# Kernel tuning notes

Hardware: AMD Instinct MI355X
Metric: run time of the kernel (lower is better)

Reference implementation:

```python
import jax, jax.numpy as jnp
import numpy as np

NHOP = 3

def setup_inputs() -> dict:
    key = jax.random.key(0)
    kq, kk, kv, kw, kb = jax.random.split(key, 5)
    B, Lq, Lk, D = 16, 512, 2048, 1024
    Q = jax.random.normal(kq, (B, Lq, D), dtype=jnp.float32)
    K = jax.random.normal(kk, (B, Lk, D), dtype=jnp.float32)
    V = jax.random.normal(kv, (B, Lk, D), dtype=jnp.float32)
    # nn.Linear(2D, D): weight [D, 2D], bias [D]
    W = jax.random.normal(kw, (D, 2 * D), dtype=jnp.float32) * (1.0 / np.sqrt(2 * D))
    b = jax.random.normal(kb, (D,), dtype=jnp.float32) * 0.01
    return {"Q": Q, "K": K, "V": V, "W": W, "b": b}


def reference(Q, K, V, W, b):
    D = Q.shape[-1]
    scale = 1.0 / jnp.sqrt(jnp.asarray(D, dtype=Q.dtype))
    Q_hop = Q
    attn = None
    for _ in range(NHOP):
        # [B, Lq, Lk]
        scores = jnp.einsum("bqd,bkd->bqk", Q_hop, K) * scale
        attn = jax.nn.softmax(scores, axis=-1)
        R = jnp.einsum("bqk,bkd->bqd", attn, V)          # [B, Lq, D]
        cat = jnp.concatenate([Q_hop, R], axis=-1)       # [B, Lq, 2D]
        Q_hop = jnp.tanh(jnp.einsum("bqe,de->bqd", cat, W) + b)
    return (Q_hop, attn)
```

## Files before the change

### kernel.cpp

```cpp
#include <hip/hip_runtime.h>
#include <math.h>

#define NB 16
#define LQ 512
#define LKK 2048
#define DD 1024

typedef _Float16 half8 __attribute__((ext_vector_type(8)));
typedef _Float16 half4 __attribute__((ext_vector_type(4)));
typedef float f32x4 __attribute__((ext_vector_type(4)));

__device__ __forceinline__ void gl_lds16(const void* g, void* l) {
    __builtin_amdgcn_global_load_lds(
        (const __attribute__((address_space(1))) void*)g,
        (__attribute__((address_space(3))) void*)l, 16, 0, 0);
}

__global__ __launch_bounds__(512, 2) void gemm_qk_256(
    const _Float16* __restrict__ A, long sA,
    const _Float16* __restrict__ B, long sB,
    _Float16* __restrict__ P, long sP,
    float* __restrict__ partial,
    float scale)
{
    __shared__ _Float16 lsA[2][256 * 64];
    __shared__ _Float16 lsB[2][256 * 64];
    const int tid = threadIdx.x;
    const int w = tid >> 6, l = tid & 63;
    const int wr = w >> 2, wc = w & 3;
    const int lrg = l >> 4, lc = l & 15, lr = lrg << 2;

    int id = blockIdx.x + gridDim.x * (blockIdx.y + gridDim.y * blockIdx.z);
    const int nwg = gridDim.x * gridDim.y * gridDim.z;
    id = (id & 7) * (nwg >> 3) + (id >> 3);
    const int bx = id % gridDim.x;
    const int t2 = id / gridDim.x;
    const int by = t2 % gridDim.y;
    const int z  = t2 / gridDim.y;
    const int m0 = by * 256, n0 = bx * 256;

    const _Float16* Ab = A + (size_t)z * sA + (size_t)m0 * DD;
    const _Float16* Bb = B + (size_t)z * sB + (size_t)n0 * DD;

    const int srow = l >> 3;
    const int sk = ((l & 7) ^ srow) << 3;

#define STG(dst, srcbase)                                                     \
    do {                                                                      \
        _Pragma("unroll")                                                     \
        for (int rr = 0; rr < 2; ++rr) {                                      \
            const int c = w + 8 * rr;                                         \
            gl_lds16((srcbase) + (size_t)(c * 8 + srow) * DD + sk,            \
                     (dst) + c * 512);                                        \
        }                                                                     \
    } while (0)

    half8 af[4][2], bf01[2][2], bf23[2][2];
    f32x4 acc[8][4] = {};
    const int rsb = (lc & 7) << 4;

#define LDA(buf, mh)                                                          \
    do {                                                                      \
        const char* p_ = (const char*)lsA[buf];                               \
        _Pragma("unroll")                                                     \
        for (int ii = 0; ii < 4; ++ii) {                                      \
            const int row_ = wr * 128 + (mh) * 64 + ii * 16 + lc;             \
            _Pragma("unroll")                                                 \
            for (int kk = 0; kk < 2; ++kk)                                    \
                af[ii][kk] = *(const half8*)(p_ + row_ * 128 +                \
                             ((kk * 64 + (lrg << 4)) ^ rsb));                 \
        }                                                                     \
    } while (0)

#define LDB(buf, nh, bfr)                                                     \
    do {                                                                      \
        const char* p_ = (const char*)lsB[buf];                               \
        _Pragma("unroll")                                                     \
        for (int jj = 0; jj < 2; ++jj) {                                      \
            const int row_ = wc * 64 + ((nh) * 2 + jj) * 16 + lc;             \
            _Pragma("unroll")                                                 \
            for (int kk = 0; kk < 2; ++kk)                                    \
                bfr[jj][kk] = *(const half8*)(p_ + row_ * 128 +               \
                              ((kk * 64 + (lrg << 4)) ^ rsb));                \
        }                                                                     \
    } while (0)

#define MM(mh, nh, bfr)                                                       \
    do {                                                                      \
        __builtin_amdgcn_s_setprio(1);                                        \
        _Pragma("unroll")                                                     \
        for (int ii = 0; ii < 4; ++ii)                                        \
            _Pragma("unroll")                                                 \
            for (int jj = 0; jj < 2; ++jj)                                    \
                _Pragma("unroll")                                             \
                for (int kk = 0; kk < 2; ++kk)                                \
                    acc[(mh) * 4 + ii][(nh) * 2 + jj] =                       \
                        __builtin_amdgcn_mfma_f32_16x16x32_f16(               \
                            af[ii][kk], bfr[jj][kk],                          \
                            acc[(mh) * 4 + ii][(nh) * 2 + jj], 0, 0, 0);      \
        __builtin_amdgcn_s_setprio(0);                                        \
    } while (0)

#define BAR __builtin_amdgcn_s_barrier()
#define VMW(n) asm volatile("s_waitcnt vmcnt(" #n ")" ::: "memory")

    STG(&lsA[0][0], Ab);
    STG(&lsA[0][128 * 64], Ab + (size_t)128 * DD);
    STG(&lsB[0][0], Bb);
    STG(&lsB[0][128 * 64], Bb + (size_t)128 * DD);
    STG(&lsA[1][0], Ab + 64);
    VMW(2);
    BAR;

    for (int i = 0; i < 7; ++i) {
        const int kt1 = (2 * i + 1) * 64, kt2 = kt1 + 64, kt3 = kt2 + 64;
        LDA(0, 0); LDB(0, 0, bf01);
        STG(&lsA[1][128 * 64], Ab + (size_t)128 * DD + kt1);
        BAR; MM(0, 0, bf01); BAR;
        LDB(0, 1, bf23);
        STG(&lsB[1][0], Bb + kt1);
        BAR; MM(0, 1, bf23); BAR;
        LDA(0, 1);
        STG(&lsB[1][128 * 64], Bb + (size_t)128 * DD + kt1);
        BAR; MM(1, 0, bf01); BAR;
        STG(&lsA[0][0], Ab + kt2);
        BAR; MM(1, 1, bf23);
        VMW(2); BAR;
        LDA(1, 0); LDB(1, 0, bf01);
        STG(&lsA[0][128 * 64], Ab + (size_t)128 * DD + kt2);
        BAR; MM(0, 0, bf01); BAR;
        LDB(1, 1, bf23);
        STG(&lsB[0][0], Bb + kt2);
        BAR; MM(0, 1, bf23); BAR;
        LDA(1, 1);
        STG(&lsB[0][128 * 64], Bb + (size_t)128 * DD + kt2);
        BAR; MM(1, 0, bf01); BAR;
        STG(&lsA[1][0], Ab + kt3);
        BAR; MM(1, 1, bf23);
        VMW(2); BAR;
    }
    {
        const int kt1 = 15 * 64;
        LDA(0, 0); LDB(0, 0, bf01);
        STG(&lsA[1][128 * 64], Ab + (size_t)128 * DD + kt1);
        BAR; MM(0, 0, bf01); BAR;
        LDB(0, 1, bf23);
        STG(&lsB[1][0], Bb + kt1);
        BAR; MM(0, 1, bf23); BAR;
        LDA(0, 1);
        STG(&lsB[1][128 * 64], Bb + (size_t)128 * DD + kt1);
        BAR; MM(1, 0, bf01); BAR;
        BAR; MM(1, 1, bf23);
        VMW(0); BAR;
        LDA(1, 0); LDB(1, 0, bf01);
        BAR; MM(0, 0, bf01); BAR;
        LDB(1, 1, bf23);
        BAR; MM(0, 1, bf23); BAR;
        LDA(1, 1);
        BAR; MM(1, 0, bf01); BAR;
        BAR; MM(1, 1, bf23);
    }
    __syncthreads();

    _Float16* Cb = P + (size_t)z * sP;
    float* psum = (float*)&lsA[0][0];
    #pragma unroll
    for (int i = 0; i < 8; ++i) {
        float rsum[4] = {0.f, 0.f, 0.f, 0.f};
        #pragma unroll
        for (int j = 0; j < 4; ++j) {
            const int n = n0 + wc * 64 + j * 16 + lc;
            #pragma unroll
            for (int r = 0; r < 4; ++r) {
                const int m = m0 + wr * 128 + i * 16 + lr + r;
                const float e = __expf(acc[i][j][r] * scale);
                Cb[(size_t)m * LKK + n] = (_Float16)e;
                rsum[r] += e;
            }
        }
        #pragma unroll
        for (int r = 0; r < 4; ++r) {
            float s = rsum[r];
            s += __shfl_xor(s, 1);
            s += __shfl_xor(s, 2);
            s += __shfl_xor(s, 4);
            s += __shfl_xor(s, 8);
            if (lc == 0) psum[(wr * 128 + i * 16 + lr + r) * 4 + wc] = s;
        }
    }
    __syncthreads();
    if (tid < 256) {
        const float* pr = psum + tid * 4;
        partial[((size_t)z * LQ + m0 + tid) * 8 + bx] = pr[0] + pr[1] + pr[2] + pr[3];
    }
#undef STG
#undef LDA
#undef LDB
#undef MM
#undef BAR
#undef VMW
}

__global__ __launch_bounds__(256) void gemm_f16_nt(
    const _Float16* __restrict__ Alo, long sAlo, int lda_lo,
    const _Float16* __restrict__ Ahi, long sAhi, int lda_hi,
    int ksplit,
    const _Float16* __restrict__ B, long sB, int ldb,
    int K, int mode, float scale,
    float* __restrict__ out32, long s32, int ldc32,
    _Float16* __restrict__ out16, long s16, int ldc16,
    const float* __restrict__ bias,
    float* __restrict__ partial, const float* __restrict__ inv, int npart)
{
    __shared__ _Float16 lsA[128 * 64];
    __shared__ _Float16 lsB[128 * 64];
    __shared__ float psum[128][2];
    const int tid = threadIdx.x;
    const int w = tid >> 6, l = tid & 63;
    const int wr = w >> 1, wc = w & 1;

    int id = blockIdx.x + gridDim.x * (blockIdx.y + gridDim.y * blockIdx.z);
    const int nwg = gridDim.x * gridDim.y * gridDim.z;
    id = (id & 7) * (nwg >> 3) + (id >> 3);
    const int bx = id % gridDim.x;
    const int t2 = id / gridDim.x;
    const int by = t2 % gridDim.y;
    const int z = t2 / gridDim.y;
    const int m0 = by * 128, n0 = bx * 128;

    const _Float16* Abase_lo = Alo + (size_t)z * sAlo + (size_t)m0 * lda_lo;
    const _Float16* Abase_hi = Ahi ? (Ahi + (size_t)z * sAhi + (size_t)m0 * lda_hi) : (const _Float16*)0;
    const _Float16* Bbase = B + (size_t)z * sB + (size_t)n0 * ldb;

    const int srow = l >> 3;
    const int sswz = ((l & 7) ^ srow) << 3;

    f32x4 acc[4][4] = {};

    for (int k0 = 0; k0 < K; k0 += 64) {
        const _Float16* Ap; int kloc, ldaA;
        if (k0 < ksplit) { Ap = Abase_lo; kloc = k0;          ldaA = lda_lo; }
        else             { Ap = Abase_hi; kloc = k0 - ksplit; ldaA = lda_hi; }
        #pragma unroll
        for (int i = 0; i < 4; ++i) {
            const int c = w * 4 + i;
            const int row = c * 8 + srow;
            gl_lds16(Ap + (size_t)row * ldaA + kloc + sswz, &lsA[c * 512]);
        }
        #pragma unroll
        for (int i = 0; i < 4; ++i) {
            const int c = w * 4 + i;
            const int row = c * 8 + srow;
            gl_lds16(Bbase + (size_t)row * ldb + k0 + sswz, &lsB[c * 512]);
        }
        __syncthreads();

        half8 af[4][2], bf[4][2];
        const char* lA = (const char*)lsA;
        const char* lB = (const char*)lsB;
        const int rs = (l & 7) << 4;
        const int cb = (l >> 4) << 4;
        #pragma unroll
        for (int i = 0; i < 4; ++i) {
            const int rowa = wr * 64 + i * 16 + (l & 15);
            const int rowb = wc * 64 + i * 16 + (l & 15);
            #pragma unroll
            for (int kk = 0; kk < 2; ++kk) {
                af[i][kk] = *(const half8*)(lA + rowa * 128 + ((kk * 64 + cb) ^ rs));
                bf[i][kk] = *(const half8*)(lB + rowb * 128 + ((kk * 64 + cb) ^ rs));
            }
        }
        #pragma unroll
        for (int kk = 0; kk < 2; ++kk)
            #pragma unroll
            for (int i = 0; i < 4; ++i)
                #pragma unroll
                for (int j = 0; j < 4; ++j)
                    acc[i][j] = __builtin_amdgcn_mfma_f32_16x16x32_f16(
                        af[i][kk], bf[j][kk], acc[i][j], 0, 0, 0);
        __syncthreads();
    }

    const int lr = (l >> 4) * 4;
    const int lc = l & 15;
    if (mode == 0) {
        _Float16* Cb = out16 + (size_t)z * s16;
        float rsum[4][4];
        #pragma unroll
        for (int i = 0; i < 4; ++i)
            #pragma unroll
            for (int r = 0; r < 4; ++r) rsum[i][r] = 0.0f;
        #pragma unroll
        for (int i = 0; i < 4; ++i)
            #pragma unroll
            for (int j = 0; j < 4; ++j) {
                const int n = n0 + wc * 64 + j * 16 + lc;
                #pragma unroll
                for (int r = 0; r < 4; ++r) {
                    const int m = m0 + wr * 64 + i * 16 + lr + r;
                    const float e = __expf(acc[i][j][r] * scale);
                    Cb[(size_t)m * ldc16 + n] = (_Float16)e;
                    rsum[i][r] += e;
                }
            }
        #pragma unroll
        for (int i = 0; i < 4; ++i)
            #pragma unroll
            for (int r = 0; r < 4; ++r) {
                float s = rsum[i][r];
                s += __shfl_xor(s, 1);
                s += __shfl_xor(s, 2);
                s += __shfl_xor(s, 4);
                s += __shfl_xor(s, 8);
                rsum[i][r] = s;
            }
        if (lc == 0) {
            #pragma unroll
            for (int i = 0; i < 4; ++i)
                #pragma unroll
                for (int r = 0; r < 4; ++r)
                    psum[wr * 64 + i * 16 + lr + r][wc] = rsum[i][r];
        }
        __syncthreads();
        if (tid < 128)
            partial[((size_t)z * LQ + m0 + tid) * npart + bx] = psum[tid][0] + psum[tid][1];
    } else if (mode == 1) {
        _Float16* Cb = out16 + (size_t)z * s16;
        float iv[4][4];
        if (partial) {
            if (tid < 128) {
                const float* pp = partial + ((size_t)z * LQ + m0 + tid) * npart;
                float s = 0.0f;
                for (int c = 0; c < npart; ++c) s += pp[c];
                psum[tid][0] = 1.0f / s;
            }
            __syncthreads();
            #pragma unroll
            for (int i = 0; i < 4; ++i)
                #pragma unroll
                for (int r = 0; r < 4; ++r)
                    iv[i][r] = psum[wr * 64 + i * 16 + lr + r][0];
        } else {
            #pragma unroll
            for (int i = 0; i < 4; ++i)
                #pragma unroll
                for (int r = 0; r < 4; ++r)
                    iv[i][r] = inv ? inv[(size_t)z * LQ + m0 + wr * 64 + i * 16 + lr + r] : 1.0f;
        }
        #pragma unroll
        for (int i = 0; i < 4; ++i)
            #pragma unroll
            for (int j = 0; j < 4; ++j) {
                const int n = n0 + wc * 64 + j * 16 + lc;
                #pragma unroll
                for (int r = 0; r < 4; ++r) {
                    const int m = m0 + wr * 64 + i * 16 + lr + r;
                    Cb[(size_t)m * ldc16 + n] = (_Float16)(acc[i][j][r] * iv[i][r]);
                }
            }
    } else if (mode == 4) {
        float* Cb = out32 + (size_t)z * s32;
        #pragma unroll
        for (int i = 0; i < 4; ++i)
            #pragma unroll
            for (int j = 0; j < 4; ++j) {
                const int n = n0 + wc * 64 + j * 16 + lc;
                #pragma unroll
                for (int r = 0; r < 4; ++r) {
                    const int m = m0 + wr * 64 + i * 16 + lr + r;
                    Cb[(size_t)m * ldc32 + n] = acc[i][j][r] * scale;
                }
            }
    } else {
        float bv[4];
        #pragma unroll
        for (int j = 0; j < 4; ++j)
            bv[j] = bias[n0 + wc * 64 + j * 16 + lc];
        #pragma unroll
        for (int i = 0; i < 4; ++i)
            #pragma unroll
            for (int j = 0; j < 4; ++j) {
                const int n = n0 + wc * 64 + j * 16 + lc;
                #pragma unroll
                for (int r = 0; r < 4; ++r) {
                    const int m = m0 + wr * 64 + i * 16 + lr + r;
                    const float t = tanhf(acc[i][j][r] + bv[j]);
                    if (out16) out16[(size_t)z * s16 + (size_t)m * ldc16 + n] = (_Float16)t;
                    if (out32) out32[(size_t)z * s32 + (size_t)m * ldc32 + n] = t;
                }
            }
    }
}

__global__ __launch_bounds__(256) void scale_attn(
    const _Float16* __restrict__ P, const float* __restrict__ partial,
    float* __restrict__ attn, int npart)
{
    __shared__ float sinv;
    const long row = blockIdx.x;
    const int tid = threadIdx.x;
    if (tid < npart) {
        float s = partial[row * npart + tid];
        for (int off = npart >> 1; off > 0; off >>= 1) s += __shfl_xor(s, off);
        if (tid == 0) sinv = 1.0f / s;
    }
    __syncthreads();
    const float inv = sinv;
    const half8 h = *(const half8*)(P + row * 2048 + tid * 8);
    float* o = attn + row * 2048 + tid * 8;
    float4 a = make_float4((float)h[0] * inv, (float)h[1] * inv,
                           (float)h[2] * inv, (float)h[3] * inv);
    float4 b = make_float4((float)h[4] * inv, (float)h[5] * inv,
                           (float)h[6] * inv, (float)h[7] * inv);
    *(float4*)o = a;
    *(float4*)(o + 4) = b;
}

__global__ __launch_bounds__(256) void make_inv(
    const float* __restrict__ partial, float* __restrict__ inv)
{
    const int row = blockIdx.x * 256 + threadIdx.x;
    const float4 a = *(const float4*)(partial + (size_t)row * 16);
    const float4 b = *(const float4*)(partial + (size_t)row * 16 + 4);
    const float4 c = *(const float4*)(partial + (size_t)row * 16 + 8);
    const float4 d = *(const float4*)(partial + (size_t)row * 16 + 12);
    const float s = (a.x + a.y + a.z + a.w) + (b.x + b.y + b.z + b.w)
                  + (c.x + c.y + c.z + c.w) + (d.x + d.y + d.z + d.w);
    inv[row] = 1.0f / s;
}

__global__ __launch_bounds__(256) void softmax_rows2(
    float* __restrict__ S, _Float16* __restrict__ f16out,
    long f16stride, int write_f32)
{
    __shared__ float red[8];
    const long row = blockIdx.x;
    float* p = S + row * LKK;
    const int tid = threadIdx.x;
    float4 v0 = ((const float4*)p)[tid];
    float4 v1 = ((const float4*)p)[tid + 256];
    float m = fmaxf(fmaxf(fmaxf(v0.x, v0.y), fmaxf(v0.z, v0.w)),
                    fmaxf(fmaxf(v1.x, v1.y), fmaxf(v1.z, v1.w)));
    #pragma unroll
    for (int off = 32; off > 0; off >>= 1) m = fmaxf(m, __shfl_down(m, off));
    if ((tid & 63) == 0) red[tid >> 6] = m;
    __syncthreads();
    m = fmaxf(fmaxf(red[0], red[1]), fmaxf(red[2], red[3]));
    v0.x = expf(v0.x - m); v0.y = expf(v0.y - m);
    v0.z = expf(v0.z - m); v0.w = expf(v0.w - m);
    v1.x = expf(v1.x - m); v1.y = expf(v1.y - m);
    v1.z = expf(v1.z - m); v1.w = expf(v1.w - m);
    float s = v0.x + v0.y + v0.z + v0.w + v1.x + v1.y + v1.z + v1.w;
    #pragma unroll
    for (int off = 32; off > 0; off >>= 1) s += __shfl_down(s, off);
    if ((tid & 63) == 0) red[4 + (tid >> 6)] = s;
    __syncthreads();
    s = red[4] + red[5] + red[6] + red[7];
    const float inv = 1.0f / s;
    v0.x *= inv; v0.y *= inv; v0.z *= inv; v0.w *= inv;
    v1.x *= inv; v1.y *= inv; v1.z *= inv; v1.w *= inv;
    if (write_f32) {
        ((float4*)p)[tid] = v0;
        ((float4*)p)[tid + 256] = v1;
    }
    _Float16* q = f16out + row * f16stride;
    half4 h0 = { (_Float16)v0.x, (_Float16)v0.y, (_Float16)v0.z, (_Float16)v0.w };
    half4 h1 = { (_Float16)v1.x, (_Float16)v1.y, (_Float16)v1.z, (_Float16)v1.w };
    *(half4*)(q + tid * 4) = h0;
    *(half4*)(q + 1024 + tid * 4) = h1;
}

__global__ __launch_bounds__(256) void cvt_f32_to_f16(
    const float* __restrict__ in, _Float16* __restrict__ out, long n)
{
    const long i = ((long)blockIdx.x * 256 + threadIdx.x) * 8;
    if (i + 8 > n) return;
    float4 a = *(const float4*)(in + i);
    float4 b = *(const float4*)(in + i + 4);
    half8 h = { (_Float16)a.x, (_Float16)a.y, (_Float16)a.z, (_Float16)a.w,
                (_Float16)b.x, (_Float16)b.y, (_Float16)b.z, (_Float16)b.w };
    *(half8*)(out + i) = h;
}

__global__ __launch_bounds__(256) void transpose_cvt_v(
    const float* __restrict__ V, _Float16* __restrict__ Vt)
{
    __shared__ _Float16 t[64][80];
    const int z = blockIdx.z;
    const int k0 = blockIdx.y * 64, d0 = blockIdx.x * 64;
    const float* Vb = V + (size_t)z * LKK * DD;
    _Float16* Vtb = Vt + (size_t)z * DD * LKK;
    const int r = threadIdx.x >> 2;
    const int c0 = (threadIdx.x & 3) * 16;
    #pragma unroll
    for (int j = 0; j < 4; ++j) {
        float4 v = *(const float4*)(Vb + (size_t)(k0 + r) * DD + d0 + c0 + j * 4);
        t[c0 + j * 4 + 0][r] = (_Float16)v.x;
        t[c0 + j * 4 + 1][r] = (_Float16)v.y;
        t[c0 + j * 4 + 2][r] = (_Float16)v.z;
        t[c0 + j * 4 + 3][r] = (_Float16)v.w;
    }
    __syncthreads();
    #pragma unroll
    for (int j = 0; j < 2; ++j) {
        half8 h = *(const half8*)&t[r][c0 + j * 8];
        *(half8*)(Vtb + (size_t)(d0 + r) * LKK + k0 + c0 + j * 8) = h;
    }
}

constexpr int TM = 64, TN = 64, TK = 32;
constexpr int PAD = 4;

__global__ __launch_bounds__(256) void gemm_nt_k(
    const float* __restrict__ A, int lda, long sA,
    const float* __restrict__ Bt, int ldb, long sB,
    float* __restrict__ C, int ldc, long sC, int K, float scale)
{
    __shared__ float As[TK][TM + PAD];
    __shared__ float Bs[TK][TN + PAD];
    const float* Ab = A + (long)blockIdx.z * sA;
    const float* Bb = Bt + (long)blockIdx.z * sB;
    float* Cb = C + (long)blockIdx.z * sC;
    const int m0 = blockIdx.y * TM, n0 = blockIdx.x * TN;
    const int tid = threadIdx.x;
    const int tn = tid & 15, tm = tid >> 4;
    float acc[4][4] = {};
    for (int k0 = 0; k0 < K; k0 += TK) {
        #pragma unroll
        for (int c = tid; c < (TM * TK) / 4; c += 256) {
            const int row = c >> 3, kc = (c & 7) << 2;
            const float4 g = *(const float4*)(Ab + (long)(m0 + row) * lda + (k0 + kc));
            As[kc + 0][row] = g.x; As[kc + 1][row] = g.y;
            As[kc + 2][row] = g.z; As[kc + 3][row] = g.w;
        }
        #pragma unroll
        for (int c = tid; c < (TN * TK) / 4; c += 256) {
            const int row = c >> 3, kc = (c & 7) << 2;
            const float4 g = *(const float4*)(Bb + (long)(n0 + row) * ldb + (k0 + kc));
            Bs[kc + 0][row] = g.x; Bs[kc + 1][row] = g.y;
            Bs[kc + 2][row] = g.z; Bs[kc + 3][row] = g.w;
        }
        __syncthreads();
        #pragma unroll
        for (int kk = 0; kk < TK; ++kk) {
            const float4 av = *(const float4*)&As[kk][tm << 2];
            const float4 bv = *(const float4*)&Bs[kk][tn << 2];
            const float a[4] = {av.x, av.y, av.z, av.w};
            const float b[4] = {bv.x, bv.y, bv.z, bv.w};
            #pragma unroll
            for (int i = 0; i < 4; ++i)
                #pragma unroll
                for (int j = 0; j < 4; ++j)
                    acc[i][j] = fmaf(a[i], b[j], acc[i][j]);
        }
        __syncthreads();
    }
    #pragma unroll
    for (int i = 0; i < 4; ++i) {
        float4 o = make_float4(acc[i][0] * scale, acc[i][1] * scale,
                               acc[i][2] * scale, acc[i][3] * scale);
        *(float4*)(Cb + (long)(m0 + (tm << 2) + i) * ldc + n0 + (tn << 2)) = o;
    }
}

__global__ __launch_bounds__(256) void gemm_nn_k(
    const float* __restrict__ A, int lda, long sA,
    const float* __restrict__ B, int ldb, long sB,
    float* __restrict__ C, int ldc, long sC, int K)
{
    __shared__ float As[TK][TM + PAD];
    __shared__ float Bs[TK][TN + PAD];
    const float* Ab = A + (long)blockIdx.z * sA;
    const float* Bb = B + (long)blockIdx.z * sB;
    float* Cb = C + (long)blockIdx.z * sC;
    const int m0 = blockIdx.y * TM, n0 = blockIdx.x * TN;
    const int tid = threadIdx.x;
    const int tn = tid & 15, tm = tid >> 4;
    float acc[4][4] = {};
    for (int k0 = 0; k0 < K; k0 += TK) {
        #pragma unroll
        for (int c = tid; c < (TM * TK) / 4; c += 256) {
            const int row = c >> 3, kc = (c & 7) << 2;
            const float4 g = *(const float4*)(Ab + (long)(m0 + row) * lda + (k0 + kc));
            As[kc + 0][row] = g.x; As[kc + 1][row] = g.y;
            As[kc + 2][row] = g.z; As[kc + 3][row] = g.w;
        }
        #pragma unroll
        for (int c = tid; c < (TK * TN) / 4; c += 256) {
            const int krow = c >> 4, nc = (c & 15) << 2;
            *(float4*)&Bs[krow][nc] =
                *(const float4*)(Bb + (long)(k0 + krow) * ldb + n0 + nc);
        }
        __syncthreads();
        #pragma unroll
        for (int kk = 0; kk < TK; ++kk) {
            const float4 av = *(const float4*)&As[kk][tm << 2];
            const float4 bv = *(const float4*)&Bs[kk][tn << 2];
            const float a[4] = {av.x, av.y, av.z, av.w};
            const float b[4] = {bv.x, bv.y, bv.z, bv.w};
            #pragma unroll
            for (int i = 0; i < 4; ++i)
                #pragma unroll
                for (int j = 0; j < 4; ++j)
                    acc[i][j] = fmaf(a[i], b[j], acc[i][j]);
        }
        __syncthreads();
    }
    #pragma unroll
    for (int i = 0; i < 4; ++i) {
        float4 o = make_float4(acc[i][0], acc[i][1], acc[i][2], acc[i][3]);
        *(float4*)(Cb + (long)(m0 + (tm << 2) + i) * ldc + n0 + (tn << 2)) = o;
    }
}

__global__ __launch_bounds__(256) void gemm_cat_k(
    const float* __restrict__ Qh, const float* __restrict__ R,
    const float* __restrict__ W, const float* __restrict__ bias,
    float* __restrict__ C)
{
    __shared__ float As[TK][TM + PAD];
    __shared__ float Bs[TK][TN + PAD];
    const float* Qb = Qh + (long)blockIdx.z * LQ * DD;
    const float* Rb = R + (long)blockIdx.z * LQ * DD;
    float* Cb = C + (long)blockIdx.z * LQ * DD;
    const int m0 = blockIdx.y * TM, n0 = blockIdx.x * TN;
    const int tid = threadIdx.x;
    const int tn = tid & 15, tm = tid >> 4;
    float acc[4][4] = {};
    for (int k0 = 0; k0 < 2 * DD; k0 += TK) {
        const float* src = (k0 < DD) ? Qb : Rb;
        const int kb = (k0 < DD) ? k0 : k0 - DD;
        #pragma unroll
        for (int c = tid; c < (TM * TK) / 4; c += 256) {
            const int row = c >> 3, kc = (c & 7) << 2;
            const float4 g = *(const float4*)(src + (long)(m0 + row) * DD + (kb + kc));
            As[kc + 0][row] = g.x; As[kc + 1][row] = g.y;
            As[kc + 2][row] = g.z; As[kc + 3][row] = g.w;
        }
        #pragma unroll
        for (int c = tid; c < (TN * TK) / 4; c += 256) {
            const int row = c >> 3, kc = (c & 7) << 2;
            const float4 g = *(const float4*)(W + (long)(n0 + row) * (2 * DD) + (k0 + kc));
            Bs[kc + 0][row] = g.x; Bs[kc + 1][row] = g.y;
            Bs[kc + 2][row] = g.z; Bs[kc + 3][row] = g.w;
        }
        __syncthreads();
        #pragma unroll
        for (int kk = 0; kk < TK; ++kk) {
            const float4 av = *(const float4*)&As[kk][tm << 2];
            const float4 bv = *(const float4*)&Bs[kk][tn << 2];
            const float a[4] = {av.x, av.y, av.z, av.w};
            const float b[4] = {bv.x, bv.y, bv.z, bv.w};
            #pragma unroll
            for (int i = 0; i < 4; ++i)
                #pragma unroll
                for (int j = 0; j < 4; ++j)
                    acc[i][j] = fmaf(a[i], b[j], acc[i][j]);
        }
        __syncthreads();
    }
    #pragma unroll
    for (int i = 0; i < 4; ++i) {
        float4 o;
        o.x = tanhf(acc[i][0] + bias[n0 + (tn << 2) + 0]);
        o.y = tanhf(acc[i][1] + bias[n0 + (tn << 2) + 1]);
        o.z = tanhf(acc[i][2] + bias[n0 + (tn << 2) + 2]);
        o.w = tanhf(acc[i][3] + bias[n0 + (tn << 2) + 3]);
        *(float4*)(Cb + (long)(m0 + (tm << 2) + i) * DD + n0 + (tn << 2)) = o;
    }
}

__global__ __launch_bounds__(256) void softmax_rows(float* __restrict__ S) {
    __shared__ float red[8];
    float* p = S + (size_t)blockIdx.x * LKK;
    const int tid = threadIdx.x;
    float4 v0 = ((const float4*)p)[tid];
    float4 v1 = ((const float4*)p)[tid + 256];
    float m = fmaxf(fmaxf(fmaxf(v0.x, v0.y), fmaxf(v0.z, v0.w)),
                    fmaxf(fmaxf(v1.x, v1.y), fmaxf(v1.z, v1.w)));
    #pragma unroll
    for (int off = 32; off > 0; off >>= 1) m = fmaxf(m, __shfl_down(m, off));
    if ((tid & 63) == 0) red[tid >> 6] = m;
    __syncthreads();
    m = fmaxf(fmaxf(red[0], red[1]), fmaxf(red[2], red[3]));
    v0.x = expf(v0.x - m); v0.y = expf(v0.y - m);
    v0.z = expf(v0.z - m); v0.w = expf(v0.w - m);
    v1.x = expf(v1.x - m); v1.y = expf(v1.y - m);
    v1.z = expf(v1.z - m); v1.w = expf(v1.w - m);
    float s = v0.x + v0.y + v0.z + v0.w + v1.x + v1.y + v1.z + v1.w;
    #pragma unroll
    for (int off = 32; off > 0; off >>= 1) s += __shfl_down(s, off);
    if ((tid & 63) == 0) red[4 + (tid >> 6)] = s;
    __syncthreads();
    s = red[4] + red[5] + red[6] + red[7];
    const float inv = 1.0f / s;
    v0.x *= inv; v0.y *= inv; v0.z *= inv; v0.w *= inv;
    v1.x *= inv; v1.y *= inv; v1.z *= inv; v1.w *= inv;
    ((float4*)p)[tid] = v0;
    ((float4*)p)[tid + 256] = v1;
}

extern "C" void kernel_launch(void* const* d_in, const int* in_sizes, int n_in,
                              void* d_out, int out_size, void* d_ws, size_t ws_size,
                              hipStream_t stream) {
    const float* Q    = (const float*)d_in[0];
    const float* Km   = (const float*)d_in[1];
    const float* V    = (const float*)d_in[2];
    const float* W    = (const float*)d_in[3];
    const float* bias = (const float*)d_in[4];
    const float scale = 0.03125f;
    dim3 blk(256);

    const size_t NEED_FULL = 189267968ULL;
    const size_t NEED_R3   = 155189248ULL;

    if (ws_size >= NEED_FULL) {
        char* ws = (char*)d_ws;
        _Float16* Kh     = (_Float16*)ws;
        _Float16* Vt     = (_Float16*)(ws + 67108864);
        _Float16* Wh     = (_Float16*)(ws + 134217728);
        _Float16* Rh     = (_Float16*)(ws + 138412032);
        _Float16* Qping  = (_Float16*)(ws + 155189248);
        _Float16* Qpong  = (_Float16*)(ws + 171966464);
        float*    partialB = (float*)(ws + 188743680);

        float*    outQ  = (float*)d_out;
        _Float16* P2    = (_Float16*)d_out;
        float*    attnF = (float*)((char*)d_out + 33554432);
        _Float16* P01   = (_Float16*)attnF;

        cvt_f32_to_f16<<<4096, blk, 0, stream>>>(Q, Qping, (long)NB * LQ * DD);
        cvt_f32_to_f16<<<16384, blk, 0, stream>>>(Km, Kh, (long)NB * LKK * DD);
        cvt_f32_to_f16<<<1024, blk, 0, stream>>>(W, Wh, (long)DD * 2 * DD);
        transpose_cvt_v<<<dim3(DD / 64, LKK / 64, NB), blk, 0, stream>>>(V, Vt);

        dim3 gS2(LKK / 256, LQ / 256, NB);
        dim3 gR(DD / 128, LQ / 128, NB);

        for (int h = 0; h < 3; ++h) {
            _Float16* qcur = (h == 1) ? Qpong : Qping;
            _Float16* P    = (h == 2) ? P2 : P01;

            gemm_qk_256<<<gS2, dim3(512), 0, stream>>>(
                qcur, (long)LQ * DD, Kh, (long)LKK * DD,
                P, (long)LQ * LKK, partialB, scale);
            if (h == 2)
                scale_attn<<<NB * LQ, blk, 0, stream>>>(P2, partialB, attnF, 8);
            gemm_f16_nt<<<gR, blk, 0, stream>>>(
                P, (long)LQ * LKK, LKK,
                (const _Float16*)0, 0, 0, LKK,
                Vt, (long)DD * LKK, LKK, LKK,
                1, 1.0f, (float*)0, 0, 0,
                Rh, (long)LQ * DD, DD, (const float*)0,
                partialB, (const float*)0, 8);
            _Float16* qn = (h == 0) ? Qpong : (h == 1) ? Qping : (_Float16*)0;
            float* fo = (h == 2) ? outQ : (float*)0;
            gemm_f16_nt<<<gR, blk, 0, stream>>>(
                qcur, (long)LQ * DD, DD,
                Rh, (long)LQ * DD, DD, DD,
                Wh, 0, 2 * DD, 2 * DD,
                2, 1.0f, fo, (long)LQ * DD, DD,
                qn, (long)LQ * DD, DD, bias,
                (float*)0, (const float*)0, 0);
        }
    } else if (ws_size >= NEED_R3) {
        char* ws = (char*)d_ws;
        _Float16* Kh  = (_Float16*)ws;
        _Float16* Vt  = (_Float16*)(ws + 67108864);
        _Float16* Wh  = (_Float16*)(ws + 134217728);
        _Float16* Rh  = (_Float16*)(ws + 138412032);
        _Float16* attn2 = (_Float16*)ws;
        float* Fout = (float*)(ws + 33554432);

        _Float16* Qping = (_Float16*)d_out;
        _Float16* Qpong = Qping + (size_t)NB * LQ * DD;
        float* S = (float*)((char*)d_out + 33554432);
        _Float16* P = (_Float16*)S;
        float* partialB = (float*)((char*)d_out + 73400320);
        float* invB     = (float*)((char*)d_out + 73924608);

        cvt_f32_to_f16<<<4096, blk, 0, stream>>>(Q, Qping, (long)NB * LQ * DD);
        cvt_f32_to_f16<<<16384, blk, 0, stream>>>(Km, Kh, (long)NB * LKK * DD);
        cvt_f32_to_f16<<<1024, blk, 0, stream>>>(W, Wh, (long)DD * 2 * DD);
        transpose_cvt_v<<<dim3(DD / 64, LKK / 64, NB), blk, 0, stream>>>(V, Vt);

        dim3 gS(LKK / 128, LQ / 128, NB);
        dim3 gR(DD / 128, LQ / 128, NB);

        for (int h = 0; h < 3; ++h) {
            _Float16* qcur = (h == 1) ? Qpong : Qping;
            if (h < 2) {
                gemm_f16_nt<<<gS, blk, 0, stream>>>(
                    qcur, (long)LQ * DD, DD, (const _Float16*)0, 0, 0, DD,
                    Kh, (long)LKK * DD, DD, DD,
                    0, scale, (float*)0, 0, 0,
                    P, (long)LQ * LKK, LKK, (const float*)0,
                    partialB, (const float*)0, 16);
                make_inv<<<32, blk, 0, stream>>>(partialB, invB);
                gemm_f16_nt<<<gR, blk, 0, stream>>>(
                    P, (long)LQ * LKK, LKK,
                    (const _Float16*)0, 0, 0, LKK,
                    Vt, (long)DD * LKK, LKK, LKK,
                    1, 1.0f, (float*)0, 0, 0,
                    Rh, (long)LQ * DD, DD, (const float*)0,
                    (float*)0, invB, 0);
            } else {
                gemm_f16_nt<<<gS, blk, 0, stream>>>(
                    qcur, (long)LQ * DD, DD, (const _Float16*)0, 0, 0, DD,
                    Kh, (long)LKK * DD, DD, DD,
                    4, scale, S, (long)LQ * LKK, LKK,
                    (_Float16*)0, 0, 0, (const float*)0,
                    (float*)0, (const float*)0, 0);
                softmax_rows2<<<NB * LQ, blk, 0, stream>>>(S, attn2, 2048L, 1);
                gemm_f16_nt<<<gR, blk, 0, stream>>>(
                    attn2, (long)LQ * LKK, LKK,
                    (const _Float16*)0, 0, 0, LKK,
                    Vt, (long)DD * LKK, LKK, LKK,
                    1, 1.0f, (float*)0, 0, 0,
                    Rh, (long)LQ * DD, DD, (const float*)0,
                    (float*)0, (const float*)0, 0);
            }
            _Float16* qn = (h == 0) ? Qpong : (h == 1) ? Qping : (_Float16*)0;
            float* fo = (h == 2) ? Fout : (float*)0;
            gemm_f16_nt<<<gR, blk, 0, stream>>>(
                qcur, (long)LQ * DD, DD,
                Rh, (long)LQ * DD, DD, DD,
                Wh, 0, 2 * DD, 2 * DD,
                2, 1.0f, fo, (long)LQ * DD, DD,
                qn, (long)LQ * DD, DD, bias,
                (float*)0, (const float*)0, 0);
        }
        hipMemcpyAsync(d_out, Fout, 33554432ULL, hipMemcpyDeviceToDevice, stream);
    } else {
        float* outQ = (float*)d_out;
        float* S    = outQ + (size_t)NB * LQ * DD;
        float* R    = (float*)d_ws;
        float* T    = R + (size_t)NB * LQ * DD;
        dim3 gS(LKK / TN, LQ / TM, NB);
        dim3 gR(DD / TN, LQ / TM, NB);
        for (int h = 0; h < 3; ++h) {
            const float* Qh = (h == 0) ? Q : (h == 1 ? (const float*)T : (const float*)outQ);
            float* cout = (h == 1) ? outQ : T;
            gemm_nt_k<<<gS, blk, 0, stream>>>(Qh, DD, (long)LQ * DD, Km, DD, (long)LKK * DD,
                                              S, LKK, (long)LQ * LKK, DD, scale);
            softmax_rows<<<NB * LQ, blk, 0, stream>>>(S);
            gemm_nn_k<<<gR, blk, 0, stream>>>(S, LKK, (long)LQ * LKK, V, DD, (long)LKK * DD,
                                              R, DD, (long)LQ * DD, LKK);
            gemm_cat_k<<<gR, blk, 0, stream>>>(Qh, R, W, bias, cout);
        }
        hipMemcpyAsync(outQ, T, (size_t)NB * LQ * DD * sizeof(float),
                       hipMemcpyDeviceToDevice, stream);
    }
}
```

Measured before the change: 536.6 us.

## Replace PV and output-projection GEMMs with 256x128 triple-buffered kernel

```diff
diff --git a/kernel.cpp b/kernel.cpp
--- a/kernel.cpp
+++ b/kernel.cpp
@@ -197,6 +197,182 @@
 #undef LDA
 #undef LDB
 #undef MM
+}
+
+__global__ __launch_bounds__(512, 2) void gemm_pc_256x128(
+    const _Float16* __restrict__ Alo, long sAlo, int lda_lo,
+    const _Float16* __restrict__ Ahi, long sAhi, int lda_hi,
+    int ksplit,
+    const _Float16* __restrict__ B, long sB, int ldb,
+    int K, int mode,
+    float* __restrict__ out32, long s32, int ldc32,
+    _Float16* __restrict__ out16, long s16, int ldc16,
+    const float* __restrict__ bias,
+    const float* __restrict__ partial, int npart)
+{
+    __shared__ _Float16 ls[3][384 * 64];
+    const int tid = threadIdx.x;
+    const int w = tid >> 6, l = tid & 63;
+    const int wr = w >> 2, wc = w & 3;
+    const int lrg = l >> 4, lc = l & 15, lr = lrg << 2;
+
+    int id = blockIdx.x + gridDim.x * (blockIdx.y + gridDim.y * blockIdx.z);
+    const int nwg = gridDim.x * gridDim.y * gridDim.z;
+    id = (id & 7) * (nwg >> 3) + (id >> 3);
+    const int bx = id % gridDim.x;
+    const int t2_ = id / gridDim.x;
+    const int by = t2_ % gridDim.y;
+    const int z  = t2_ / gridDim.y;
+    const int m0 = by * 256, n0 = bx * 128;
+
+    const _Float16* Abase_lo = Alo + (size_t)z * sAlo + (size_t)m0 * lda_lo;
+    const _Float16* Abase_hi = Ahi ? (Ahi + (size_t)z * sAhi + (size_t)m0 * lda_hi) : (const _Float16*)0;
+    const _Float16* Bbase = B + (size_t)z * sB + (size_t)n0 * ldb;
+
+    const int srow = l >> 3;
+    const int sk = ((l & 7) ^ srow) << 3;
+    const int rsb = (lc & 7) << 4;
+
+    half8 af[4][2], bf[2][2];
+    f32x4 acc[8][2] = {};
+
+#define STGA(tt, dbuf)                                                        \
+    do {                                                                      \
+        const int kb_ = (tt) * 64;                                            \
+        const _Float16* s_; int ld_;                                          \
+        if (kb_ < ksplit) { s_ = Abase_lo + kb_;           ld_ = lda_lo; }    \
+        else              { s_ = Abase_hi + (kb_ - ksplit); ld_ = lda_hi; }   \
+        _Float16* d_ = &ls[dbuf][0];                                          \
+        _Pragma("unroll")                                                     \
+        for (int rr = 0; rr < 4; ++rr) {                                      \
+            const int c = w + 8 * rr;                                         \
+            gl_lds16(s_ + (size_t)(c * 8 + srow) * ld_ + sk, d_ + c * 512);   \
+        }                                                                     \
+    } while (0)
+
+#define STGB(tt, dbuf)                                                        \
+    do {                                                                      \
+        const _Float16* s_ = Bbase + (tt) * 64;                               \
+        _Float16* d_ = &ls[dbuf][256 * 64];                                   \
+        _Pragma("unroll")                                                     \
+        for (int rr = 0; rr < 2; ++rr) {                                      \
+            const int c = w + 8 * rr;                                         \
+            gl_lds16(s_ + (size_t)(c * 8 + srow) * ldb + sk, d_ + c * 512);   \
+        }                                                                     \
+    } while (0)
+
+#define LDA2(buf, mh)                                                         \
+    do {                                                                      \
+        const char* p_ = (const char*)&ls[buf][0];                            \
+        _Pragma("unroll")                                                     \
+        for (int ii = 0; ii < 4; ++ii) {                                      \
+            const int row_ = wr * 128 + (mh) * 64 + ii * 16 + lc;             \
+            _Pragma("unroll")                                                 \
+            for (int kk = 0; kk < 2; ++kk)                                    \
+                af[ii][kk] = *(const half8*)(p_ + row_ * 128 +                \
+                             ((kk * 64 + (lrg << 4)) ^ rsb));                 \
+        }                                                                     \
+    } while (0)
+
+#define LDB2(buf)                                                             \
+    do {                                                                      \
+        const char* p_ = (const char*)&ls[buf][256 * 64];                     \
+        _Pragma("unroll")                                                     \
+        for (int jj = 0; jj < 2; ++jj) {                                      \
+            const int row_ = wc * 32 + jj * 16 + lc;                          \
+            _Pragma("unroll")                                                 \
+            for (int kk = 0; kk < 2; ++kk)                                    \
+                bf[jj][kk] = *(const half8*)(p_ + row_ * 128 +                \
+                              ((kk * 64 + (lrg << 4)) ^ rsb));                \
+        }                                                                     \
+    } while (0)
+
+#define MM2(mh)                                                               \
+    do {                                                                      \
+        __builtin_amdgcn_s_setprio(1);                                        \
+        _Pragma("unroll")                                                     \
+        for (int ii = 0; ii < 4; ++ii)                                        \
+            _Pragma("unroll")                                                 \
+            for (int jj = 0; jj < 2; ++jj)                                    \
+                _Pragma("unroll")                                             \
+                for (int kk = 0; kk < 2; ++kk)                                \
+                    acc[(mh) * 4 + ii][jj] =                                  \
+                        __builtin_amdgcn_mfma_f32_16x16x32_f16(               \
+                            af[ii][kk], bf[jj][kk],                           \
+                            acc[(mh) * 4 + ii][jj], 0, 0, 0);                 \
+        __builtin_amdgcn_s_setprio(0);                                        \
+    } while (0)
+
+    const int NT = K >> 6;
+    STGA(0, 0); STGB(0, 0);
+    STGA(1, 1); STGB(1, 1);
+    VMW(6);
+    BAR;
+
+    int b = 0, b2 = 2;
+    for (int t = 0; t < NT; ++t) {
+        const int tt = t + 2;
+        const bool st = tt < NT;
+        LDA2(b, 0); LDB2(b);
+        if (st) STGA(tt, b2);
+        BAR; MM2(0); BAR;
+        LDA2(b, 1);
+        if (st) STGB(tt, b2);
+        BAR; MM2(1);
+        if (t < NT - 2)       VMW(6);
+        else if (t == NT - 2) VMW(0);
+        BAR;
+        b = (b == 2) ? 0 : b + 1;
+        b2 = (b2 == 2) ? 0 : b2 + 1;
+    }
+    __syncthreads();
+
+    if (mode == 1) {
+        float* psum = (float*)&ls[0][0];
+        if (tid < 256) {
+            const float* pp = partial + ((size_t)z * LQ + m0 + tid) * npart;
+            float s = 0.0f;
+            for (int c = 0; c < npart; ++c) s += pp[c];
+            psum[tid] = 1.0f / s;
+        }
+        __syncthreads();
+        _Float16* Cb = out16 + (size_t)z * s16;
+        #pragma unroll
+        for (int i = 0; i < 8; ++i)
+            #pragma unroll
+            for (int j = 0; j < 2; ++j) {
+                const int n = n0 + wc * 32 + j * 16 + lc;
+                #pragma unroll
+                for (int r = 0; r < 4; ++r) {
+                    const int ml = wr * 128 + i * 16 + lr + r;
+                    Cb[(size_t)(m0 + ml) * ldc16 + n] =
+                        (_Float16)(acc[i][j][r] * psum[ml]);
+                }
+            }
+    } else {
+        float bv[2];
+        #pragma unroll
+        for (int j = 0; j < 2; ++j)
+            bv[j] = bias[n0 + wc * 32 + j * 16 + lc];
+        #pragma unroll
+        for (int i = 0; i < 8; ++i)
+            #pragma unroll
+            for (int j = 0; j < 2; ++j) {
+                const int n = n0 + wc * 32 + j * 16 + lc;
+                #pragma unroll
+                for (int r = 0; r < 4; ++r) {
+                    const int m = m0 + wr * 128 + i * 16 + lr + r;
+                    const float t = tanhf(acc[i][j][r] + bv[j]);
+                    if (out16) out16[(size_t)z * s16 + (size_t)m * ldc16 + n] = (_Float16)t;
+                    if (out32) out32[(size_t)z * s32 + (size_t)m * ldc32 + n] = t;
+                }
+            }
+    }
+#undef STGA
+#undef STGB
+#undef LDA2
+#undef LDB2
+#undef MM2
 #undef BAR
 #undef VMW
 }
@@ -735,7 +911,7 @@
         transpose_cvt_v<<<dim3(DD / 64, LKK / 64, NB), blk, 0, stream>>>(V, Vt);
 
         dim3 gS2(LKK / 256, LQ / 256, NB);
-        dim3 gR(DD / 128, LQ / 128, NB);
+        dim3 gP(DD / 128, LQ / 256, NB);
 
         for (int h = 0; h < 3; ++h) {
             _Float16* qcur = (h == 1) ? Qpong : Qping;
@@ -746,22 +922,24 @@
                 P, (long)LQ * LKK, partialB, scale);
             if (h == 2)
                 scale_attn<<<NB * LQ, blk, 0, stream>>>(P2, partialB, attnF, 8);
-            gemm_f16_nt<<<gR, blk, 0, stream>>>(
+            gemm_pc_256x128<<<gP, dim3(512), 0, stream>>>(
                 P, (long)LQ * LKK, LKK,
-                (const _Float16*)0, 0, 0, LKK,
-                Vt, (long)DD * LKK, LKK, LKK,
-                1, 1.0f, (float*)0, 0, 0,
-                Rh, (long)LQ * DD, DD, (const float*)0,
-                partialB, (const float*)0, 8);
+                (const _Float16*)0, 0, 0, LKK * 16,
+                Vt, (long)DD * LKK, LKK,
+                LKK, 1,
+                (float*)0, 0, 0,
+                Rh, (long)LQ * DD, DD,
+                (const float*)0, partialB, 8);
             _Float16* qn = (h == 0) ? Qpong : (h == 1) ? Qping : (_Float16*)0;
             float* fo = (h == 2) ? outQ : (float*)0;
-            gemm_f16_nt<<<gR, blk, 0, stream>>>(
+            gemm_pc_256x128<<<gP, dim3(512), 0, stream>>>(
                 qcur, (long)LQ * DD, DD,
                 Rh, (long)LQ * DD, DD, DD,
-                Wh, 0, 2 * DD, 2 * DD,
-                2, 1.0f, fo, (long)LQ * DD, DD,
-                qn, (long)LQ * DD, DD, bias,
-                (float*)0, (const float*)0, 0);
+                Wh, 0, 2 * DD,
+                2 * DD, 2,
+                fo, (long)LQ * DD, DD,
+                qn, (long)LQ * DD, DD,
+                bias, (const float*)0, 0);
         }
     } else if (ws_size >= NEED_R3) {
         char* ws = (char*)d_ws;
```

Measured after the change: 500.2 us. 6.8% less time.
